# Optimization experiments

Measured on AMD Instinct MI355X. Metric: run time of the kernel, lower is better.

Reference implementation:

```python
import jax, jax.numpy as jnp
import numpy as np

EPS = 1e-12  # F.normalize denominator clamp


def setup_inputs() -> dict:
    key = jax.random.key(0)
    k1, k2, k3, k4 = jax.random.split(key, 4)
    bs, d, nc, ncl, cs, ny = 8192, 768, 64, 500, 100, 1000
    train_embedding = jax.random.normal(k1, (bs, d), dtype=jnp.float32)
    clusters = jax.random.normal(k2, (ncl, cs, d), dtype=jnp.float32)
    # init_concept: uniform in [-0.5, 0.5]
    concept = jax.random.uniform(k3, (d, nc), dtype=jnp.float32, minval=-0.5, maxval=0.5)
    W_h = jax.random.normal(k4, (d, ny), dtype=jnp.float32) * 0.02
    b_h = jnp.zeros((ny,), dtype=jnp.float32)
    return {"train_embedding": train_embedding, "clusters": clusters,
            "concept": concept, "W_h": W_h, "b_h": b_h}


def reference(train_embedding, clusters, concept, W_h, b_h):
    # column-wise L2 normalize concept (F.normalize p=2 dim=0)
    concept_normalized = concept / jnp.maximum(
        jnp.linalg.norm(concept, axis=0, keepdims=True), EPS)
    # projection onto span(concept): C (C^T C)^-1 C^T
    gram = concept.T @ concept                      # [nc, nc]
    proj_matrix = concept @ jnp.linalg.inv(gram) @ concept.T  # [d, d]
    proj = proj_matrix @ train_embedding.T          # [d, bs]
    cluster_mean = jnp.mean(clusters, axis=1)       # [ncl, d]
    score_matrix = jnp.abs(cluster_mean @ concept_normalized)  # [ncl, nc]
    score_norm = score_matrix / jnp.maximum(
        jnp.linalg.norm(score_matrix, axis=0, keepdims=True), EPS)
    L_sparse_1 = jnp.sum(score_norm)
    # sum_{i != j} <score_norm[:,i], score_norm[:,j]> == sum(G) - trace(G)
    G = score_norm.T @ score_norm                   # [nc, nc]
    L_sparse_2 = jnp.sum(G) - jnp.trace(G)
    y_pred = proj.T @ W_h + b_h                     # h_x as linear head, [bs, ny]
    return (y_pred, L_sparse_1, L_sparse_2)
```

## Files before the change

kernel.cpp:

```cpp
#include <hip/hip_runtime.h>
#include <hip/hip_bf16.h>
#include <math.h>

#define BS   8192
#define DD   768
#define NC   64
#define NCL  500
#define CS   100
#define NY   1000
#define EPSN 1e-12f

typedef __attribute__((ext_vector_type(8))) short bf16x8;
typedef __attribute__((ext_vector_type(4))) float f32x4;

union B8 { unsigned u[4]; bf16x8 v; uint4 q; };

__device__ inline unsigned short f2bf(float x) {
    __hip_bfloat16 h = __float2bfloat16(x);
    return *reinterpret_cast<unsigned short*>(&h);
}
__device__ inline unsigned pk2(float a, float b) {
    return (unsigned)f2bf(a) | ((unsigned)f2bf(b) << 16);
}

#define FMA4(acc, s, v) { (acc).x = fmaf((s), (v).x, (acc).x); \
                          (acc).y = fmaf((s), (v).y, (acc).y); \
                          (acc).z = fmaf((s), (v).z, (acc).z); \
                          (acc).w = fmaf((s), (v).w, (acc).w); }

__global__ __launch_bounds__(256) void k_pre(
    const float* __restrict__ clusters, const float* __restrict__ C,
    float* __restrict__ cmP, uint4* __restrict__ Cb) {
    int b = blockIdx.x, tid = threadIdx.x;
    if (b < 1500) {
        int sp  = b & 3;
        int idx = (b >> 2) * 256 + tid;
        int r  = idx / 192;
        int d4 = idx % 192;
        const float4* base = (const float4*)clusters
                           + (size_t)r * CS * 192 + (size_t)sp * 25 * 192 + d4;
        float4 a0={0,0,0,0},a1={0,0,0,0},a2={0,0,0,0},a3={0,0,0,0},a4={0,0,0,0};
        for (int s = 0; s < 25; s += 5) {
            float4 v0 = base[(size_t)(s+0)*192];
            float4 v1 = base[(size_t)(s+1)*192];
            float4 v2 = base[(size_t)(s+2)*192];
            float4 v3 = base[(size_t)(s+3)*192];
            float4 v4 = base[(size_t)(s+4)*192];
            a0.x+=v0.x; a0.y+=v0.y; a0.z+=v0.z; a0.w+=v0.w;
            a1.x+=v1.x; a1.y+=v1.y; a1.z+=v1.z; a1.w+=v1.w;
            a2.x+=v2.x; a2.y+=v2.y; a2.z+=v2.z; a2.w+=v2.w;
            a3.x+=v3.x; a3.y+=v3.y; a3.z+=v3.z; a3.w+=v3.w;
            a4.x+=v4.x; a4.y+=v4.y; a4.z+=v4.z; a4.w+=v4.w;
        }
        float4 o;
        o.x = a0.x+a1.x+a2.x+a3.x+a4.x;
        o.y = a0.y+a1.y+a2.y+a3.y+a4.y;
        o.z = a0.z+a1.z+a2.z+a3.z+a4.z;
        o.w = a0.w+a1.w+a2.w+a3.w+a4.w;
        ((float4*)(cmP + (size_t)sp * 384000))[idx] = o;
    } else {
        int ks = b - 1500;
        int kg = tid >> 6, n = tid & 63;
        const float* cp = C + (size_t)(ks*32 + kg*8) * 64 + n;
        uint4 g;
        g.x = pk2(cp[0],     cp[64]);
        g.y = pk2(cp[2*64],  cp[3*64]);
        g.z = pk2(cp[4*64],  cp[5*64]);
        g.w = pk2(cp[6*64],  cp[7*64]);
        Cb[(ks*4 + kg)*64 + n] = g;
    }
}

__global__ __launch_bounds__(256) void k_gemms(
    const float* __restrict__ C, const float* __restrict__ W,
    const float* __restrict__ X, const uint4* __restrict__ Cb,
    float* __restrict__ gramP, float* __restrict__ Up,
    unsigned short* __restrict__ Tb) {
    __shared__ __align__(16) char smem_raw[25600];
    int b = blockIdx.x, tid = threadIdx.x;

    if (b < 128) {
        int r0 = b * 64;
        int w  = tid >> 6, l = tid & 63;
        int rowA = r0 + w*16 + (l & 15);
        int kq   = l >> 4;
        const float* xb = X + (size_t)rowA * DD + kq * 8;
        f32x4 acc[4];
        #pragma unroll
        for (int ng = 0; ng < 4; ++ng) acc[ng] = (f32x4){0.f, 0.f, 0.f, 0.f};
        #pragma unroll 2
        for (int ks = 0; ks < 24; ++ks) {
            float4 xa = *((const float4*)(xb + ks*32));
            float4 xc = *((const float4*)(xb + ks*32 + 4));
            B8 a;
            a.u[0] = pk2(xa.x, xa.y); a.u[1] = pk2(xa.z, xa.w);
            a.u[2] = pk2(xc.x, xc.y); a.u[3] = pk2(xc.z, xc.w);
            const uint4* cbase = Cb + (ks*4 + kq)*64 + (l & 15);
            B8 b0, b1, b2, b3;
            b0.q = cbase[0];  b1.q = cbase[16];
            b2.q = cbase[32]; b3.q = cbase[48];
            acc[0] = __builtin_amdgcn_mfma_f32_16x16x32_bf16(a.v, b0.v, acc[0], 0, 0, 0);
            acc[1] = __builtin_amdgcn_mfma_f32_16x16x32_bf16(a.v, b1.v, acc[1], 0, 0, 0);
            acc[2] = __builtin_amdgcn_mfma_f32_16x16x32_bf16(a.v, b2.v, acc[2], 0, 0, 0);
            acc[3] = __builtin_amdgcn_mfma_f32_16x16x32_bf16(a.v, b3.v, acc[3], 0, 0, 0);
        }
        int rw = r0 + w*16 + (l >> 4) * 4;
        #pragma unroll
        for (int ng = 0; ng < 4; ++ng) {
            int n = ng*16 + (l & 15);
            #pragma unroll
            for (int r = 0; r < 4; ++r)
                Tb[(size_t)(rw + r) * 64 + n] = f2bf(acc[ng][r]);
        }
    } else if (b < 384) {
        int q  = b - 128;
        int j  = q & 63, ks = q >> 6;
        int i   = tid & 63;
        int seg = tid >> 6;
        int k0  = ks * 192 + seg * 48;
        float p = 0.f;
        for (int k = k0; k < k0 + 48; ++k)
            p += C[k * NC + i] * C[k * NC + j];
        float (*red)[64] = (float(*)[64])smem_raw;
        red[seg][i] = p;
        __syncthreads();
        if (seg == 0)
            gramP[(size_t)ks * 4096 + i * NC + j] =
                red[0][i] + red[1][i] + red[2][i] + red[3][i];
    } else {
        int q  = b - 384;
        int nt = q >> 2, ks = q & 3;
        int n0 = nt * 128, kb = ks * 192;
        float (*Cu)[68]  = (float(*)[68])smem_raw;
        float (*Wu)[132] = (float(*)[132])(smem_raw + 8704);
        int tx = tid & 15, ty = tid >> 4;
        float4 a0[4], a1[4];
        #pragma unroll
        for (int i = 0; i < 4; ++i) { a0[i] = make_float4(0,0,0,0); a1[i] = make_float4(0,0,0,0); }
        for (int kc = kb; kc < kb + 192; kc += 32) {
            __syncthreads();
            {   int i4 = tid & 15, kk = tid >> 4;
                *((float4*)&Cu[kk][i4*4])    = *((const float4*)(C + (size_t)(kc+kk)*64 + i4*4));
                *((float4*)&Cu[kk+16][i4*4]) = *((const float4*)(C + (size_t)(kc+kk+16)*64 + i4*4));
            }
            {   int nf = tid & 31, kq2 = tid >> 5;
                #pragma unroll
                for (int u = 0; u < 4; ++u) {
                    int k = kq2 + u * 8;
                    int n = n0 + nf * 4;
                    float4 v = {0.f, 0.f, 0.f, 0.f};
                    if (n < NY) v = *((const float4*)(W + (size_t)(kc + k) * NY + n));
                    *((float4*)&Wu[k][nf*4]) = v;
                }
            }
            __syncthreads();
            #pragma unroll 8
            for (int k = 0; k < 32; ++k) {
                float4 ci = *((float4*)&Cu[k][ty*4]);
                float4 w0 = *((float4*)&Wu[k][tx*8]);
                float4 w1 = *((float4*)&Wu[k][tx*8+4]);
                FMA4(a0[0], ci.x, w0); FMA4(a1[0], ci.x, w1);
                FMA4(a0[1], ci.y, w0); FMA4(a1[1], ci.y, w1);
                FMA4(a0[2], ci.z, w0); FMA4(a1[2], ci.z, w1);
                FMA4(a0[3], ci.w, w0); FMA4(a1[3], ci.w, w1);
            }
        }
        float* Ups = Up + (size_t)ks * 64000;
        #pragma unroll
        for (int i = 0; i < 4; ++i) {
            int irow = ty * 4 + i;
            int n = n0 + tx * 8;
            if (n < NY)     *((float4*)(Ups + (size_t)irow * NY + n))     = a0[i];
            if (n + 4 < NY) *((float4*)(Ups + (size_t)irow * NY + n + 4)) = a1[i];
        }
    }
}

__global__ __launch_bounds__(256) void k_phaseB(
    const float* __restrict__ gramP, const float* __restrict__ cmP,
    const float* __restrict__ C, float* __restrict__ ginv,
    float* __restrict__ SP) {
    __shared__ __align__(16) char smem_raw[52224];
    int blk = blockIdx.x;
    int tid = threadIdx.x;
    if (blk == 0) {
        int c = tid & 63;
        int q = tid >> 6;
        float a[16], bb[16];
        #pragma unroll
        for (int i = 0; i < 16; ++i) {
            int r = q * 16 + i;
            size_t off = (size_t)r * 64 + c;
            a[i]  = gramP[off] + gramP[4096 + off] + gramP[8192 + off] + gramP[12288 + off];
            bb[i] = (r == c) ? 1.f : 0.f;
        }
        __shared__ float asr[2][64];
        __shared__ float bsr[2][64];
        for (int p = 0; p < 64; ++p) {
            int qp  = p >> 4;
            int lp  = p & 15;
            int par = p & 1;
            if (q == qp) {
                float ap = 0.f, bp = 0.f;
                #pragma unroll
                for (int i = 0; i < 16; ++i)
                    if (i == lp) { ap = a[i]; bp = bb[i]; }
                float App = __shfl(ap, p);
                float s   = 1.0f / App;
                asr[par][c] = ap * s;
                bsr[par][c] = bp * s;
            }
            __syncthreads();
            float as_ = asr[par][c];
            float bs_ = bsr[par][c];
            #pragma unroll
            for (int i = 0; i < 16; ++i) {
                float f = __shfl(a[i], p);
                bool isp = (q == qp) && (i == lp);
                a[i]  = isp ? as_ : fmaf(-f, as_, a[i]);
                bb[i] = isp ? bs_ : fmaf(-f, bs_, bb[i]);
            }
        }
        #pragma unroll
        for (int i = 0; i < 16; ++i)
            ginv[(q * 16 + i) * 64 + c] = bb[i];
    } else {
        int q = blk - 1;
        int tile = q >> 2, ks = q & 3;
        int r0 = tile * 128, kb = ks * 192;
        float (*Mr)[68] = (float(*)[68])smem_raw;
        float (*Cs)[68] = (float(*)[68])(smem_raw + 128*68*4);
        int tx = tid & 15, ty = tid >> 4;
        float4 acc[8];
        #pragma unroll
        for (int r = 0; r < 8; ++r) acc[r] = make_float4(0.f,0.f,0.f,0.f);
        for (int kc = 0; kc < 192; kc += 64) {
            __syncthreads();
            #pragma unroll
            for (int p = 0; p < 8; ++p) {
                int f = tid + p * 256;
                int row = f >> 4, k4 = f & 15;
                int gr = r0 + row;
                int grc = gr < NCL ? gr : (NCL - 1);
                size_t off = (size_t)grc*DD + kb + kc + k4*4;
                float4 c0 = *((const float4*)(cmP + off));
                float4 c1 = *((const float4*)(cmP + 384000 + off));
                float4 c2 = *((const float4*)(cmP + 768000 + off));
                float4 c3 = *((const float4*)(cmP + 1152000 + off));
                float4 m;
                m.x = (c0.x+c1.x+c2.x+c3.x) * 0.01f;
                m.y = (c0.y+c1.y+c2.y+c3.y) * 0.01f;
                m.z = (c0.z+c1.z+c2.z+c3.z) * 0.01f;
                m.w = (c0.w+c1.w+c2.w+c3.w) * 0.01f;
                *((float4*)&Mr[row][k4*4]) = m;
            }
            #pragma unroll
            for (int p = 0; p < 4; ++p) {
                int f = tid + p * 256;
                int k = f >> 4, c4 = f & 15;
                *((float4*)&Cs[k][c4*4]) =
                    *((const float4*)(C + (size_t)(kb+kc+k)*64 + c4*4));
            }
            __syncthreads();
            for (int k0 = 0; k0 < 64; k0 += 4) {
                float4 cv0 = *((float4*)&Cs[k0+0][tx*4]);
                float4 cv1 = *((float4*)&Cs[k0+1][tx*4]);
                float4 cv2 = *((float4*)&Cs[k0+2][tx*4]);
                float4 cv3 = *((float4*)&Cs[k0+3][tx*4]);
                #pragma unroll
                for (int r = 0; r < 8; ++r) {
                    float4 xv = *((float4*)&Mr[ty*8+r][k0]);
                    FMA4(acc[r], xv.x, cv0);
                    FMA4(acc[r], xv.y, cv1);
                    FMA4(acc[r], xv.z, cv2);
                    FMA4(acc[r], xv.w, cv3);
                }
            }
        }
        float* SPs = SP + (size_t)ks * 32000;
        #pragma unroll
        for (int r = 0; r < 8; ++r) {
            int row = r0 + ty * 8 + r;
            if (row < NCL)
                *((float4*)(SPs + (size_t)row * 64 + tx*4)) = acc[r];
        }
    }
}

__global__ __launch_bounds__(256) void k_vc(
    const float* __restrict__ ginv, const float* __restrict__ Up,
    float* __restrict__ SP, unsigned short* __restrict__ Vb,
    float* __restrict__ out2) {
    __shared__ __align__(16) char smem_raw[34816];
    int blk = blockIdx.x, tid = threadIdx.x;
    if (blk == 16) {
        __shared__ float colred[4][64];
        __shared__ float rn[64];
        __shared__ float trc[64];
        __shared__ float r1[4], r2[4];
        const float* SP0 = SP;
        const float* SP1 = SP + 32000;
        const float* SP2 = SP + 64000;
        const float* SP3 = SP + 96000;
        int c = tid & 63, seg = tid >> 6;
        float p = 0.f;
        for (int r = seg; r < NCL; r += 4) {
            int off = r * 64 + c;
            float s = fabsf(SP0[off] + SP1[off] + SP2[off] + SP3[off]);
            SP[off] = s;
            p += s * s;
        }
        colred[seg][c] = p;
        __syncthreads();
        if (seg == 0) {
            float n2  = colred[0][c] + colred[1][c] + colred[2][c] + colred[3][c];
            float inv = 1.0f / fmaxf(sqrtf(n2), EPSN);
            rn[c]  = inv;
            trc[c] = n2 * inv * inv;
        }
        __syncthreads();
        float l1p = 0.f, l2p = 0.f;
        for (int r = tid; r < NCL; r += 256) {
            float rs = 0.f;
            #pragma unroll
            for (int cc = 0; cc < 64; ++cc)
                rs += SP[r * 64 + cc] * rn[cc];
            l1p += rs;
            l2p += rs * rs;
        }
        #pragma unroll
        for (int off = 32; off > 0; off >>= 1) {
            l1p += __shfl_down(l1p, off);
            l2p += __shfl_down(l2p, off);
        }
        int wave = tid >> 6, lane = tid & 63;
        if (lane == 0) { r1[wave] = l1p; r2[wave] = l2p; }
        __syncthreads();
        if (tid == 0) {
            float L1 = r1[0] + r1[1] + r1[2] + r1[3];
            float L2 = r2[0] + r2[1] + r2[2] + r2[3];
            float tr = 0.f;
            #pragma unroll
            for (int cc = 0; cc < 64; ++cc) tr += trc[cc];
            out2[0] = L1;
            out2[1] = L2 - tr;
        }
        return;
    }
    float (*Us)[68] = (float(*)[68])smem_raw;
    float (*Gs)[68] = (float(*)[68])(smem_raw + 64*68*4);
    int c0 = blk * 64;
    int tx = tid & 15, ty = tid >> 4;
    const float* Up0 = Up;
    const float* Up1 = Up + 64000;
    const float* Up2 = Up + 128000;
    const float* Up3 = Up + 192000;
    #pragma unroll
    for (int p = 0; p < 4; ++p) {
        int f = tid + p * 256;
        int j = f >> 4, n4 = f & 15;
        int n = c0 + n4 * 4;
        float4 v = {0.f, 0.f, 0.f, 0.f};
        if (n < NY) {
            float4 u0 = *((const float4*)(Up0 + (size_t)j * NY + n));
            float4 u1 = *((const float4*)(Up1 + (size_t)j * NY + n));
            float4 u2 = *((const float4*)(Up2 + (size_t)j * NY + n));
            float4 u3 = *((const float4*)(Up3 + (size_t)j * NY + n));
            v.x = u0.x + u1.x + u2.x + u3.x;
            v.y = u0.y + u1.y + u2.y + u3.y;
            v.z = u0.z + u1.z + u2.z + u3.z;
            v.w = u0.w + u1.w + u2.w + u3.w;
        }
        *((float4*)&Us[j][n4*4]) = v;
        *((float4*)&Gs[j][n4*4]) = *((const float4*)(ginv + (size_t)j * 64 + n4*4));
    }
    __syncthreads();
    float4 acc[4];
    #pragma unroll
    for (int i = 0; i < 4; ++i) acc[i] = make_float4(0.f,0.f,0.f,0.f);
    for (int j0 = 0; j0 < 64; j0 += 4) {
        #pragma unroll
        for (int jj = 0; jj < 4; ++jj) {
            float4 g = *((float4*)&Gs[j0+jj][ty*4]);
            float4 u = *((float4*)&Us[j0+jj][tx*4]);
            FMA4(acc[0], g.x, u);
            FMA4(acc[1], g.y, u);
            FMA4(acc[2], g.z, u);
            FMA4(acc[3], g.w, u);
        }
    }
    #pragma unroll
    for (int i = 0; i < 4; ++i) {
        int krow = ty * 4 + i;
        Vb[(size_t)(c0 + tx*4 + 0) * 64 + krow] = f2bf(acc[i].x);
        Vb[(size_t)(c0 + tx*4 + 1) * 64 + krow] = f2bf(acc[i].y);
        Vb[(size_t)(c0 + tx*4 + 2) * 64 + krow] = f2bf(acc[i].z);
        Vb[(size_t)(c0 + tx*4 + 3) * 64 + krow] = f2bf(acc[i].w);
    }
}

__global__ __launch_bounds__(256) void k_ypred(
    const uint4* __restrict__ Tb, const uint4* __restrict__ Vbq,
    const float* __restrict__ bh, float* __restrict__ Y) {
    int blk = blockIdx.x, tid = threadIdx.x;
    int rb = blk >> 3, cb = blk & 7;
    int r0g = rb * 128, c0g = cb * 128;
    int w = tid >> 6, l = tid & 63;
    int wr = (w >> 1) * 64, wc = (w & 1) * 64;
    int kq = l >> 4, ln = l & 15;
    f32x4 acc[4][4];
    #pragma unroll
    for (int rg = 0; rg < 4; ++rg)
        #pragma unroll
        for (int ng = 0; ng < 4; ++ng) acc[rg][ng] = (f32x4){0.f,0.f,0.f,0.f};
    #pragma unroll
    for (int ks = 0; ks < 2; ++ks) {
        B8 a[4], bb[4];
        #pragma unroll
        for (int rg = 0; rg < 4; ++rg) {
            int row = r0g + wr + rg*16 + ln;
            a[rg].q = Tb[(size_t)row * 8 + ks*4 + kq];
        }
        #pragma unroll
        for (int ng = 0; ng < 4; ++ng) {
            int n = c0g + wc + ng*16 + ln;
            bb[ng].q = Vbq[(size_t)n * 8 + ks*4 + kq];
        }
        #pragma unroll
        for (int rg = 0; rg < 4; ++rg)
            #pragma unroll
            for (int ng = 0; ng < 4; ++ng)
                acc[rg][ng] = __builtin_amdgcn_mfma_f32_16x16x32_bf16(
                    a[rg].v, bb[ng].v, acc[rg][ng], 0, 0, 0);
    }
    #pragma unroll
    for (int ng = 0; ng < 4; ++ng) {
        int n = c0g + wc + ng*16 + ln;
        if (n < NY) {
            float bias = bh[n];
            #pragma unroll
            for (int rg = 0; rg < 4; ++rg) {
                int row = r0g + wr + rg*16 + kq*4;
                #pragma unroll
                for (int r = 0; r < 4; ++r)
                    Y[(size_t)(row + r) * NY + n] = acc[rg][ng][r] + bias;
            }
        }
    }
}

extern "C" void kernel_launch(void* const* d_in, const int* in_sizes, int n_in,
                              void* d_out, int out_size, void* d_ws, size_t ws_size,
                              hipStream_t stream) {
    const float* X        = (const float*)d_in[0];
    const float* clusters = (const float*)d_in[1];
    const float* C        = (const float*)d_in[2];
    const float* W        = (const float*)d_in[3];
    const float* bh       = (const float*)d_in[4];
    float* out = (float*)d_out;
    float* ws  = (float*)d_ws;

    float* cmP   = ws;
    float* gramP = cmP   + 1536000;
    float* ginv  = gramP + 16384;
    float* Up    = ginv  + 4096;
    float* SP    = Up    + 256000;
    float* CbF   = SP    + 128000;
    float* TbF   = CbF   + 24576;
    float* VbF   = TbF   + 262144;

    uint4*          Cb  = (uint4*)CbF;
    unsigned short* Tb  = (unsigned short*)TbF;
    unsigned short* Vb  = (unsigned short*)VbF;

    k_pre   <<<dim3(1524), dim3(256), 0, stream>>>(clusters, C, cmP, Cb);
    k_gemms <<<dim3(416),  dim3(256), 0, stream>>>(C, W, X, Cb, gramP, Up, Tb);
    k_phaseB<<<dim3(17),   dim3(256), 0, stream>>>(gramP, cmP, C, ginv, SP);
    k_vc    <<<dim3(17),   dim3(256), 0, stream>>>(ginv, Up, SP, Vb, out + (size_t)BS * NY);
    k_ypred <<<dim3(512),  dim3(256), 0, stream>>>((const uint4*)Tb, (const uint4*)Vb, bh, out);
}
```

Baseline: 161.6 us.

## Regroup kernel stages to cut one launch and overlap independent work

The gram-partial and C·W partial products, which depend only on the inputs, move into the first kernel next to the cluster-mean and C bf16 packing. The X·C MFMA GEMM now runs in the same launch as the 64x64 inverse and the score-partial blocks. This removes one kernel launch and its serialization bubble, and lets small dependent tasks overlap with the large T GEMM. The first kernel now reserves 25.6KB of shared memory for every block, including the reduction blocks that never use it, which may lower occupancy there. The second kernel now also mixes the single serial inverse block with the GEMM blocks and uses 52KB of shared memory.

```diff
diff --git a/kernel.cpp b/kernel.cpp
--- a/kernel.cpp
+++ b/kernel.cpp
@@ -28,9 +28,12 @@
                           (acc).z = fmaf((s), (v).z, (acc).z); \
                           (acc).w = fmaf((s), (v).w, (acc).w); }
 
-__global__ __launch_bounds__(256) void k_pre(
+__global__ __launch_bounds__(256) void k_front(
     const float* __restrict__ clusters, const float* __restrict__ C,
-    float* __restrict__ cmP, uint4* __restrict__ Cb) {
+    const float* __restrict__ W, float* __restrict__ cmP,
+    uint4* __restrict__ Cb, float* __restrict__ gramP,
+    float* __restrict__ Up) {
+    __shared__ __align__(16) char smem_raw[25600];
     int b = blockIdx.x, tid = threadIdx.x;
     if (b < 1500) {
         int sp  = b & 3;
@@ -58,7 +61,7 @@
         o.z = a0.z+a1.z+a2.z+a3.z+a4.z;
         o.w = a0.w+a1.w+a2.w+a3.w+a4.w;
         ((float4*)(cmP + (size_t)sp * 384000))[idx] = o;
-    } else {
+    } else if (b < 1524) {
         int ks = b - 1500;
         int kg = tid >> 6, n = tid & 63;
         const float* cp = C + (size_t)(ks*32 + kg*8) * 64 + n;
@@ -68,17 +71,77 @@
         g.z = pk2(cp[4*64],  cp[5*64]);
         g.w = pk2(cp[6*64],  cp[7*64]);
         Cb[(ks*4 + kg)*64 + n] = g;
-    }
-}
-
-__global__ __launch_bounds__(256) void k_gemms(
-    const float* __restrict__ C, const float* __restrict__ W,
+    } else if (b < 1780) {
+        int q  = b - 1524;
+        int j  = q & 63, ks = q >> 6;
+        int i   = tid & 63;
+        int seg = tid >> 6;
+        int k0  = ks * 192 + seg * 48;
+        float p = 0.f;
+        for (int k = k0; k < k0 + 48; ++k)
+            p += C[k * NC + i] * C[k * NC + j];
+        float (*red)[64] = (float(*)[64])smem_raw;
+        red[seg][i] = p;
+        __syncthreads();
+        if (seg == 0)
+            gramP[(size_t)ks * 4096 + i * NC + j] =
+                red[0][i] + red[1][i] + red[2][i] + red[3][i];
+    } else {
+        int q  = b - 1780;
+        int nt = q >> 2, ks = q & 3;
+        int n0 = nt * 128, kb = ks * 192;
+        float (*Cu)[68]  = (float(*)[68])smem_raw;
+        float (*Wu)[132] = (float(*)[132])(smem_raw + 8704);
+        int tx = tid & 15, ty = tid >> 4;
+        float4 a0[4], a1[4];
+        #pragma unroll
+        for (int i = 0; i < 4; ++i) { a0[i] = make_float4(0,0,0,0); a1[i] = make_float4(0,0,0,0); }
+        for (int kc = kb; kc < kb + 192; kc += 32) {
+            __syncthreads();
+            {   int i4 = tid & 15, kk = tid >> 4;
+                *((float4*)&Cu[kk][i4*4])    = *((const float4*)(C + (size_t)(kc+kk)*64 + i4*4));
+                *((float4*)&Cu[kk+16][i4*4]) = *((const float4*)(C + (size_t)(kc+kk+16)*64 + i4*4));
+            }
+            {   int nf = tid & 31, kq2 = tid >> 5;
+                #pragma unroll
+                for (int u = 0; u < 4; ++u) {
+                    int k = kq2 + u * 8;
+                    int n = n0 + nf * 4;
+                    float4 v = {0.f, 0.f, 0.f, 0.f};
+                    if (n < NY) v = *((const float4*)(W + (size_t)(kc + k) * NY + n));
+                    *((float4*)&Wu[k][nf*4]) = v;
+                }
+            }
+            __syncthreads();
+            #pragma unroll 8
+            for (int k = 0; k < 32; ++k) {
+                float4 ci = *((float4*)&Cu[k][ty*4]);
+                float4 w0 = *((float4*)&Wu[k][tx*8]);
+                float4 w1 = *((float4*)&Wu[k][tx*8+4]);
+                FMA4(a0[0], ci.x, w0); FMA4(a1[0], ci.x, w1);
+                FMA4(a0[1], ci.y, w0); FMA4(a1[1], ci.y, w1);
+                FMA4(a0[2], ci.z, w0); FMA4(a1[2], ci.z, w1);
+                FMA4(a0[3], ci.w, w0); FMA4(a1[3], ci.w, w1);
+            }
+        }
+        float* Ups = Up + (size_t)ks * 64000;
+        #pragma unroll
+        for (int i = 0; i < 4; ++i) {
+            int irow = ty * 4 + i;
+            int n = n0 + tx * 8;
+            if (n < NY)     *((float4*)(Ups + (size_t)irow * NY + n))     = a0[i];
+            if (n + 4 < NY) *((float4*)(Ups + (size_t)irow * NY + n + 4)) = a1[i];
+        }
+    }
+}
+
+__global__ __launch_bounds__(256) void k_mid(
     const float* __restrict__ X, const uint4* __restrict__ Cb,
-    float* __restrict__ gramP, float* __restrict__ Up,
-    unsigned short* __restrict__ Tb) {
-    __shared__ __align__(16) char smem_raw[25600];
+    const float* __restrict__ gramP, const float* __restrict__ cmP,
+    const float* __restrict__ C, unsigned short* __restrict__ Tb,
+    float* __restrict__ ginv, float* __restrict__ SP) {
+    __shared__ __align__(16) char smem_raw[52224];
     int b = blockIdx.x, tid = threadIdx.x;
-
     if (b < 128) {
         int r0 = b * 64;
         int w  = tid >> 6, l = tid & 63;
@@ -112,78 +175,7 @@
             for (int r = 0; r < 4; ++r)
                 Tb[(size_t)(rw + r) * 64 + n] = f2bf(acc[ng][r]);
         }
-    } else if (b < 384) {
-        int q  = b - 128;
-        int j  = q & 63, ks = q >> 6;
-        int i   = tid & 63;
-        int seg = tid >> 6;
-        int k0  = ks * 192 + seg * 48;
-        float p = 0.f;
-        for (int k = k0; k < k0 + 48; ++k)
-            p += C[k * NC + i] * C[k * NC + j];
-        float (*red)[64] = (float(*)[64])smem_raw;
-        red[seg][i] = p;
-        __syncthreads();
-        if (seg == 0)
-            gramP[(size_t)ks * 4096 + i * NC + j] =
-                red[0][i] + red[1][i] + red[2][i] + red[3][i];
-    } else {
-        int q  = b - 384;
-        int nt = q >> 2, ks = q & 3;
-        int n0 = nt * 128, kb = ks * 192;
-        float (*Cu)[68]  = (float(*)[68])smem_raw;
-        float (*Wu)[132] = (float(*)[132])(smem_raw + 8704);
-        int tx = tid & 15, ty = tid >> 4;
-        float4 a0[4], a1[4];
-        #pragma unroll
-        for (int i = 0; i < 4; ++i) { a0[i] = make_float4(0,0,0,0); a1[i] = make_float4(0,0,0,0); }
-        for (int kc = kb; kc < kb + 192; kc += 32) {
-            __syncthreads();
-            {   int i4 = tid & 15, kk = tid >> 4;
-                *((float4*)&Cu[kk][i4*4])    = *((const float4*)(C + (size_t)(kc+kk)*64 + i4*4));
-                *((float4*)&Cu[kk+16][i4*4]) = *((const float4*)(C + (size_t)(kc+kk+16)*64 + i4*4));
-            }
-            {   int nf = tid & 31, kq2 = tid >> 5;
-                #pragma unroll
-                for (int u = 0; u < 4; ++u) {
-                    int k = kq2 + u * 8;
-                    int n = n0 + nf * 4;
-                    float4 v = {0.f, 0.f, 0.f, 0.f};
-                    if (n < NY) v = *((const float4*)(W + (size_t)(kc + k) * NY + n));
-                    *((float4*)&Wu[k][nf*4]) = v;
-                }
-            }
-            __syncthreads();
-            #pragma unroll 8
-            for (int k = 0; k < 32; ++k) {
-                float4 ci = *((float4*)&Cu[k][ty*4]);
-                float4 w0 = *((float4*)&Wu[k][tx*8]);
-                float4 w1 = *((float4*)&Wu[k][tx*8+4]);
-                FMA4(a0[0], ci.x, w0); FMA4(a1[0], ci.x, w1);
-                FMA4(a0[1], ci.y, w0); FMA4(a1[1], ci.y, w1);
-                FMA4(a0[2], ci.z, w0); FMA4(a1[2], ci.z, w1);
-                FMA4(a0[3], ci.w, w0); FMA4(a1[3], ci.w, w1);
-            }
-        }
-        float* Ups = Up + (size_t)ks * 64000;
-        #pragma unroll
-        for (int i = 0; i < 4; ++i) {
-            int irow = ty * 4 + i;
-            int n = n0 + tx * 8;
-            if (n < NY)     *((float4*)(Ups + (size_t)irow * NY + n))     = a0[i];
-            if (n + 4 < NY) *((float4*)(Ups + (size_t)irow * NY + n + 4)) = a1[i];
-        }
-    }
-}
-
-__global__ __launch_bounds__(256) void k_phaseB(
-    const float* __restrict__ gramP, const float* __restrict__ cmP,
-    const float* __restrict__ C, float* __restrict__ ginv,
-    float* __restrict__ SP) {
-    __shared__ __align__(16) char smem_raw[52224];
-    int blk = blockIdx.x;
-    int tid = threadIdx.x;
-    if (blk == 0) {
+    } else if (b == 128) {
         int c = tid & 63;
         int q = tid >> 6;
         float a[16], bb[16];
@@ -225,7 +217,7 @@
         for (int i = 0; i < 16; ++i)
             ginv[(q * 16 + i) * 64 + c] = bb[i];
     } else {
-        int q = blk - 1;
+        int q = b - 129;
         int tile = q >> 2, ks = q & 3;
         int r0 = tile * 128, kb = ks * 192;
         float (*Mr)[68] = (float(*)[68])smem_raw;
@@ -473,9 +465,8 @@
     unsigned short* Tb  = (unsigned short*)TbF;
     unsigned short* Vb  = (unsigned short*)VbF;
 
-    k_pre   <<<dim3(1524), dim3(256), 0, stream>>>(clusters, C, cmP, Cb);
-    k_gemms <<<dim3(416),  dim3(256), 0, stream>>>(C, W, X, Cb, gramP, Up, Tb);
-    k_phaseB<<<dim3(17),   dim3(256), 0, stream>>>(gramP, cmP, C, ginv, SP);
+    k_front <<<dim3(1812), dim3(256), 0, stream>>>(clusters, C, W, cmP, Cb, gramP, Up);
+    k_mid   <<<dim3(145),  dim3(256), 0, stream>>>(X, Cb, gramP, cmP, C, Tb, ginv, SP);
     k_vc    <<<dim3(17),   dim3(256), 0, stream>>>(ginv, Up, SP, Vb, out + (size_t)BS * NY);
     k_ypred <<<dim3(512),  dim3(256), 0, stream>>>((const uint4*)Tb, (const uint4*)Vb, bh, out);
 }
```

New measurement: 158.1 us. 1.02x faster.

## Fuse pre-pass and GEMM kernels into one front kernel with in-block concept packing

Applied to the files above, without the earlier changes.

Merges k_pre and k_gemms into a single k_front launch. The X·C GEMM blocks now convert the concept matrix to bf16 themselves, staging it in shared memory per 64-wide k chunk instead of reading a packed global copy. This removes one kernel launch and its dependency barrier, and lets the cluster-mean reduction run concurrently with the GEMMs. In exchange, every GEMM block redoes the concept conversion and adds two __syncthreads per k chunk.

```diff
diff --git a/kernel.cpp b/kernel.cpp
--- a/kernel.cpp
+++ b/kernel.cpp
@@ -28,13 +28,68 @@
                           (acc).z = fmaf((s), (v).z, (acc).z); \
                           (acc).w = fmaf((s), (v).w, (acc).w); }
 
-__global__ __launch_bounds__(256) void k_pre(
+__global__ __launch_bounds__(256) void k_front(
     const float* __restrict__ clusters, const float* __restrict__ C,
-    float* __restrict__ cmP, uint4* __restrict__ Cb) {
+    const float* __restrict__ W, const float* __restrict__ X,
+    float* __restrict__ cmP, float* __restrict__ gramP,
+    float* __restrict__ Up, unsigned short* __restrict__ Tb) {
+    __shared__ __align__(16) char smem_raw[25600];
     int b = blockIdx.x, tid = threadIdx.x;
-    if (b < 1500) {
-        int sp  = b & 3;
-        int idx = (b >> 2) * 256 + tid;
+    if (b < 128) {
+        uint4 (*CbL)[64] = (uint4(*)[64])smem_raw;
+        int r0 = b * 64;
+        int w  = tid >> 6, l = tid & 63;
+        int rowA = r0 + w*16 + (l & 15);
+        int kq   = l >> 4;
+        const float* xb = X + (size_t)rowA * DD + kq * 8;
+        f32x4 acc[4];
+        #pragma unroll
+        for (int ng = 0; ng < 4; ++ng) acc[ng] = (f32x4){0.f, 0.f, 0.f, 0.f};
+        for (int kc = 0; kc < DD; kc += 64) {
+            __syncthreads();
+            #pragma unroll
+            for (int u = 0; u < 2; ++u) {
+                int g = (tid >> 6) + u*4;
+                int n = tid & 63;
+                const float* cp = C + (size_t)(kc + g*8) * 64 + n;
+                uint4 gr;
+                gr.x = pk2(cp[0],   cp[64]);
+                gr.y = pk2(cp[128], cp[192]);
+                gr.z = pk2(cp[256], cp[320]);
+                gr.w = pk2(cp[384], cp[448]);
+                CbL[g][n] = gr;
+            }
+            __syncthreads();
+            #pragma unroll
+            for (int ks2 = 0; ks2 < 2; ++ks2) {
+                float4 xa = *((const float4*)(xb + kc + ks2*32));
+                float4 xc = *((const float4*)(xb + kc + ks2*32 + 4));
+                B8 a;
+                a.u[0] = pk2(xa.x, xa.y); a.u[1] = pk2(xa.z, xa.w);
+                a.u[2] = pk2(xc.x, xc.y); a.u[3] = pk2(xc.z, xc.w);
+                B8 b0, b1, b2, b3;
+                b0.q = CbL[ks2*4 + kq][(l & 15)];
+                b1.q = CbL[ks2*4 + kq][(l & 15) + 16];
+                b2.q = CbL[ks2*4 + kq][(l & 15) + 32];
+                b3.q = CbL[ks2*4 + kq][(l & 15) + 48];
+                acc[0] = __builtin_amdgcn_mfma_f32_16x16x32_bf16(a.v, b0.v, acc[0], 0, 0, 0);
+                acc[1] = __builtin_amdgcn_mfma_f32_16x16x32_bf16(a.v, b1.v, acc[1], 0, 0, 0);
+                acc[2] = __builtin_amdgcn_mfma_f32_16x16x32_bf16(a.v, b2.v, acc[2], 0, 0, 0);
+                acc[3] = __builtin_amdgcn_mfma_f32_16x16x32_bf16(a.v, b3.v, acc[3], 0, 0, 0);
+            }
+        }
+        int rw = r0 + w*16 + kq * 4;
+        #pragma unroll
+        for (int ng = 0; ng < 4; ++ng) {
+            int n = ng*16 + (l & 15);
+            #pragma unroll
+            for (int r = 0; r < 4; ++r)
+                Tb[(size_t)(rw + r) * 64 + n] = f2bf(acc[ng][r]);
+        }
+    } else if (b < 1628) {
+        int q   = b - 128;
+        int sp  = q & 3;
+        int idx = (q >> 2) * 256 + tid;
         int r  = idx / 192;
         int d4 = idx % 192;
         const float4* base = (const float4*)clusters
@@ -58,62 +113,8 @@
         o.z = a0.z+a1.z+a2.z+a3.z+a4.z;
         o.w = a0.w+a1.w+a2.w+a3.w+a4.w;
         ((float4*)(cmP + (size_t)sp * 384000))[idx] = o;
-    } else {
-        int ks = b - 1500;
-        int kg = tid >> 6, n = tid & 63;
-        const float* cp = C + (size_t)(ks*32 + kg*8) * 64 + n;
-        uint4 g;
-        g.x = pk2(cp[0],     cp[64]);
-        g.y = pk2(cp[2*64],  cp[3*64]);
-        g.z = pk2(cp[4*64],  cp[5*64]);
-        g.w = pk2(cp[6*64],  cp[7*64]);
-        Cb[(ks*4 + kg)*64 + n] = g;
-    }
-}
-
-__global__ __launch_bounds__(256) void k_gemms(
-    const float* __restrict__ C, const float* __restrict__ W,
-    const float* __restrict__ X, const uint4* __restrict__ Cb,
-    float* __restrict__ gramP, float* __restrict__ Up,
-    unsigned short* __restrict__ Tb) {
-    __shared__ __align__(16) char smem_raw[25600];
-    int b = blockIdx.x, tid = threadIdx.x;
-
-    if (b < 128) {
-        int r0 = b * 64;
-        int w  = tid >> 6, l = tid & 63;
-        int rowA = r0 + w*16 + (l & 15);
-        int kq   = l >> 4;
-        const float* xb = X + (size_t)rowA * DD + kq * 8;
-        f32x4 acc[4];
-        #pragma unroll
-        for (int ng = 0; ng < 4; ++ng) acc[ng] = (f32x4){0.f, 0.f, 0.f, 0.f};
-        #pragma unroll 2
-        for (int ks = 0; ks < 24; ++ks) {
-            float4 xa = *((const float4*)(xb + ks*32));
-            float4 xc = *((const float4*)(xb + ks*32 + 4));
-            B8 a;
-            a.u[0] = pk2(xa.x, xa.y); a.u[1] = pk2(xa.z, xa.w);
-            a.u[2] = pk2(xc.x, xc.y); a.u[3] = pk2(xc.z, xc.w);
-            const uint4* cbase = Cb + (ks*4 + kq)*64 + (l & 15);
-            B8 b0, b1, b2, b3;
-            b0.q = cbase[0];  b1.q = cbase[16];
-            b2.q = cbase[32]; b3.q = cbase[48];
-            acc[0] = __builtin_amdgcn_mfma_f32_16x16x32_bf16(a.v, b0.v, acc[0], 0, 0, 0);
-            acc[1] = __builtin_amdgcn_mfma_f32_16x16x32_bf16(a.v, b1.v, acc[1], 0, 0, 0);
-            acc[2] = __builtin_amdgcn_mfma_f32_16x16x32_bf16(a.v, b2.v, acc[2], 0, 0, 0);
-            acc[3] = __builtin_amdgcn_mfma_f32_16x16x32_bf16(a.v, b3.v, acc[3], 0, 0, 0);
-        }
-        int rw = r0 + w*16 + (l >> 4) * 4;
-        #pragma unroll
-        for (int ng = 0; ng < 4; ++ng) {
-            int n = ng*16 + (l & 15);
-            #pragma unroll
-            for (int r = 0; r < 4; ++r)
-                Tb[(size_t)(rw + r) * 64 + n] = f2bf(acc[ng][r]);
-        }
-    } else if (b < 384) {
-        int q  = b - 128;
+    } else if (b < 1884) {
+        int q  = b - 1628;
         int j  = q & 63, ks = q >> 6;
         int i   = tid & 63;
         int seg = tid >> 6;
@@ -128,7 +129,7 @@
             gramP[(size_t)ks * 4096 + i * NC + j] =
                 red[0][i] + red[1][i] + red[2][i] + red[3][i];
     } else {
-        int q  = b - 384;
+        int q  = b - 1884;
         int nt = q >> 2, ks = q & 3;
         int n0 = nt * 128, kb = ks * 192;
         float (*Cu)[68]  = (float(*)[68])smem_raw;
@@ -176,13 +177,12 @@
     }
 }
 
-__global__ __launch_bounds__(256) void k_phaseB(
+__global__ __launch_bounds__(256) void k_mid(
     const float* __restrict__ gramP, const float* __restrict__ cmP,
     const float* __restrict__ C, float* __restrict__ ginv,
     float* __restrict__ SP) {
     __shared__ __align__(16) char smem_raw[52224];
-    int blk = blockIdx.x;
-    int tid = threadIdx.x;
+    int blk = blockIdx.x, tid = threadIdx.x;
     if (blk == 0) {
         int c = tid & 63;
         int q = tid >> 6;
@@ -465,17 +465,14 @@
     float* ginv  = gramP + 16384;
     float* Up    = ginv  + 4096;
     float* SP    = Up    + 256000;
-    float* CbF   = SP    + 128000;
-    float* TbF   = CbF   + 24576;
+    float* TbF   = SP    + 128000;
     float* VbF   = TbF   + 262144;
 
-    uint4*          Cb  = (uint4*)CbF;
     unsigned short* Tb  = (unsigned short*)TbF;
     unsigned short* Vb  = (unsigned short*)VbF;
 
-    k_pre   <<<dim3(1524), dim3(256), 0, stream>>>(clusters, C, cmP, Cb);
-    k_gemms <<<dim3(416),  dim3(256), 0, stream>>>(C, W, X, Cb, gramP, Up, Tb);
-    k_phaseB<<<dim3(17),   dim3(256), 0, stream>>>(gramP, cmP, C, ginv, SP);
+    k_front <<<dim3(1916), dim3(256), 0, stream>>>(clusters, C, W, X, cmP, gramP, Up, Tb);
+    k_mid   <<<dim3(17),   dim3(256), 0, stream>>>(gramP, cmP, C, ginv, SP);
     k_vc    <<<dim3(17),   dim3(256), 0, stream>>>(ginv, Up, SP, Vb, out + (size_t)BS * NY);
     k_ypred <<<dim3(512),  dim3(256), 0, stream>>>((const uint4*)Tb, (const uint4*)Vb, bh, out);
 }
```

Result: no change. 161.0 us (-0.3%).
